# Performance work log

Hardware: AMD Instinct MI355X
Metric: run time of the kernel (lower is better)

The kernel has to match this reference:

```python
import jax, jax.numpy as jnp
import numpy as np
from jax import lax

WS = 32          # region_size
N = WS * WS      # tokens per region = 1024
H = 8            # num_heads
HD = 64          # head_dim
C = H * HD       # dim = 512
B = 8            # num_regions * batch
K = 15           # conv_k
SCALE = HD ** -0.5


def _rel_index():
    # Swin relative position index, computed statically with numpy.
    coords = np.stack(np.meshgrid(np.arange(WS), np.arange(WS), indexing='ij'))  # [2,WS,WS]
    flat = coords.reshape(2, -1)                                                 # [2,N]
    rel = (flat[:, :, None] - flat[:, None, :]).transpose(1, 2, 0)               # [N,N,2]
    rel = rel.copy()
    rel[..., 0] += WS - 1
    rel[..., 1] += WS - 1
    rel[..., 0] *= 2 * WS - 1
    return rel.sum(-1)  # [N,N] int

_REL_IDX = jnp.asarray(_rel_index())


def setup_inputs() -> dict:
    key = jax.random.key(0)
    ks = jax.random.split(key, 6)
    return {
        'x': jax.random.normal(ks[0], (B, N, C), dtype=jnp.float32),
        'w_qkv': jax.random.normal(ks[1], (3 * C, C), dtype=jnp.float32) * 0.02,
        'b_qkv': jnp.zeros((3 * C,), dtype=jnp.float32),
        'w_proj': jax.random.normal(ks[2], (C, C), dtype=jnp.float32) * 0.02,
        'b_proj': jnp.zeros((C,), dtype=jnp.float32),
        'rel_table': jax.random.normal(ks[3], ((2 * WS - 1) ** 2, H), dtype=jnp.float32) * 0.02,
        'pe_w': jax.random.normal(ks[4], (H, 1, K, 1), dtype=jnp.float32) * 0.02,
        'pe_b': jnp.zeros((H,), dtype=jnp.float32),
    }


def reference(x, w_qkv, b_qkv, w_proj, b_proj, rel_table, pe_w, pe_b):
    b, n, c = x.shape
    qkv = (x @ w_qkv.T + b_qkv).reshape(b, n, 3, H, HD)
    q = jnp.moveaxis(qkv[:, :, 0], 2, 1)  # [B,H,N,HD]
    k = jnp.moveaxis(qkv[:, :, 1], 2, 1)
    v = jnp.moveaxis(qkv[:, :, 2], 2, 1)

    attn = jnp.einsum('bhnd,bhmd->bhnm', q * SCALE, k)  # [B,H,N,N]

    # depthwise (per-head) conv over the query axis of the attention matrix, kernel (K,1)
    pe = lax.conv_general_dilated(
        attn, pe_w, window_strides=(1, 1), padding=[(K // 2, K // 2), (0, 0)],
        dimension_numbers=('NCHW', 'OIHW', 'NCHW'), feature_group_count=H,
    ) + pe_b[None, :, None, None]
    attn = attn + pe

    # relative position bias gather: [N*N] -> [N,N,H] -> [H,N,N]
    bias = rel_table[_REL_IDX.reshape(-1)].reshape(n, n, H).transpose(2, 0, 1)
    attn = jax.nn.softmax(attn + bias[None], axis=-1)

    out = jnp.einsum('bhnm,bhmd->bnhd', attn, v).reshape(b, n, c)
    return out @ w_proj.T + b_proj
```

## Files before the change

kernel.cpp:

```cpp
#include <hip/hip_runtime.h>

typedef __bf16 bf16x8 __attribute__((ext_vector_type(8)));
typedef float f32x4 __attribute__((ext_vector_type(4)));
typedef unsigned short u16;
typedef unsigned int u32;
typedef unsigned long long u64;

__device__ __forceinline__ float bf2f(u16 x){ u32 u = ((u32)x)<<16; return __builtin_bit_cast(float,u); }
__device__ __forceinline__ u16 f2bf(float f){ u32 u = __builtin_bit_cast(u32,f); u = (u + 0x7fffu + ((u>>16)&1u)) >> 16; return (u16)u; }

__device__ __forceinline__ void glds16(const u16* g, u16* l){
  __builtin_amdgcn_global_load_lds((const __attribute__((address_space(1))) u32*)g,
                                   (__attribute__((address_space(3))) u32*)l, 16, 0, 0);
}

static constexpr float L2E = 1.4426950408889634f;
static constexpr float QSC = 0.125f * 1.4426950408889634f;

__global__ void k_cvtall(const float* __restrict__ x, const float* __restrict__ wq,
                         const float* __restrict__ wp, const float* __restrict__ rt,
                         u16* __restrict__ xo, u16* __restrict__ wqo,
                         u16* __restrict__ wpo, u64* __restrict__ rel2){
  int bid = blockIdx.x;
  if (bid < 5120){
    int i = bid*256 + threadIdx.x;
    const float* s; u16* d; int base;
    if (i < 1048576){ s=x; d=xo; base=0; }
    else if (i < 1245184){ s=wq; d=wqo; base=1048576; }
    else { s=wp; d=wpo; base=1245184; }
    int j = i - base;
    float4 v = reinterpret_cast<const float4*>(s)[j];
    reinterpret_cast<ushort4*>(d)[j] = make_ushort4(f2bf(v.x),f2bf(v.y),f2bf(v.z),f2bf(v.w));
  } else {
    int i = (bid-5120)*256 + threadIdx.x;
    if (i < 31752){
      int h = i / 3969, i2 = i - h*3969;
      u64 v = 0;
      #pragma unroll
      for (int j=0;j<4;j++){
        int idx = i2-3+j;
        u16 bb = 0;
        if (idx >= 0) bb = f2bf(rt[idx*8+h]*L2E);
        v |= (u64)bb << (16*j);
      }
      rel2[i] = v;
    }
  }
}

__device__ __forceinline__ void acc8(float* acc, uint4 v, float w){
  acc[0]=fmaf(w, bf2f((u16)(v.x)),     acc[0]); acc[1]=fmaf(w, bf2f((u16)(v.x>>16)), acc[1]);
  acc[2]=fmaf(w, bf2f((u16)(v.y)),     acc[2]); acc[3]=fmaf(w, bf2f((u16)(v.y>>16)), acc[3]);
  acc[4]=fmaf(w, bf2f((u16)(v.z)),     acc[4]); acc[5]=fmaf(w, bf2f((u16)(v.z>>16)), acc[5]);
  acc[6]=fmaf(w, bf2f((u16)(v.w)),     acc[6]); acc[7]=fmaf(w, bf2f((u16)(v.w>>16)), acc[7]);
}

template<int MODE>
__global__ __launch_bounds__(256) void k_gemm(
  const u16* __restrict__ A, const u16* __restrict__ Bw, const float* __restrict__ bias,
  u16* __restrict__ qo, u16* __restrict__ ko, u16* __restrict__ vo, float* __restrict__ co)
{
  constexpr int K = 512;
  constexpr int BM = (MODE==0) ? 128 : 64;
  constexpr int NX = (MODE==0) ? 12 : 4;
  constexpr int CPX = NX*(8192/BM)/8;
  constexpr int NF = (MODE==0) ? 4 : 2;
  __shared__ __align__(16) u16 lA[3][BM*32];
  __shared__ __align__(16) u16 lB[3][4096];
  const int lin = blockIdx.y*NX + blockIdx.x;
  const int swz = (lin&7)*CPX + (lin>>3);
  const int i0 = (swz/NX)*BM, j0 = (swz%NX)*128;
  const int T = threadIdx.x;
  const int w = T>>6, lane = T&63, g = lane>>4, cl = lane&15;
  const int wr = (MODE==0) ? (w>>1)*64 : 0;
  const int wc = (MODE==0) ? (w&1)*64 : w*32;
  const int sr = T>>2, sk = 8*(T&3);
  f32x4 acc[4][NF];
  #pragma unroll
  for (int a=0;a<4;a++)
    #pragma unroll
    for (int b=0;b<NF;b++) acc[a][b] = (f32x4){0.f,0.f,0.f,0.f};

  auto STAGE = [&](int t, u16* bA, u16* bB){
    glds16(A  + (long)(i0+sr)*K    + t*32 + sk, bA + 8*T);
    if (MODE==0) glds16(A + (long)(i0+64+sr)*K + t*32 + sk, bA + 2048 + 8*T);
    glds16(Bw + (long)(j0+sr)*K    + t*32 + sk, bB + 8*T);
    glds16(Bw + (long)(j0+64+sr)*K + t*32 + sk, bB + 2048 + 8*T);
  };
  STAGE(0, lA[0], lB[0]);
  STAGE(1, lA[1], lB[1]);
  int cur = 0, sb = 2;
  for (int t=0;t<16;t++){
    if (t<15){
      if (MODE==0) asm volatile("s_waitcnt vmcnt(4)" ::: "memory");
      else         asm volatile("s_waitcnt vmcnt(3)" ::: "memory");
    } else {
      asm volatile("s_waitcnt vmcnt(0)" ::: "memory");
    }
    __builtin_amdgcn_s_barrier();
    asm volatile("" ::: "memory");
    if (t<14) STAGE(t+2, lA[sb], lB[sb]);
    const u16* cA = lA[cur];
    const u16* cB = lB[cur];
    bf16x8 af[4], bfr[NF];
    #pragma unroll
    for (int mf=0;mf<4;mf++) af[mf]  = *reinterpret_cast<const bf16x8*>(cA + (wr+16*mf+cl)*32 + 8*g);
    #pragma unroll
    for (int nf=0;nf<NF;nf++) bfr[nf] = *reinterpret_cast<const bf16x8*>(cB + (wc+16*nf+cl)*32 + 8*g);
    __builtin_amdgcn_s_setprio(1);
    #pragma unroll
    for (int mf=0;mf<4;mf++)
      #pragma unroll
      for (int nf=0;nf<NF;nf++)
        acc[mf][nf] = __builtin_amdgcn_mfma_f32_16x16x32_bf16(af[mf], bfr[nf], acc[mf][nf], 0,0,0);
    __builtin_amdgcn_s_setprio(0);
    cur = (cur==2)?0:cur+1;
    sb  = (sb==2)?0:sb+1;
  }

  #pragma unroll
  for (int mf=0;mf<4;mf++){
    #pragma unroll
    for (int nf=0;nf<NF;nf++){
      const int col = j0 + wc + 16*nf + cl;
      const float bb = bias[col];
      const int row0 = i0 + wr + 16*mf + 4*g;
      if (MODE==0){
        const int part = col>>9, h=(col>>6)&7, dd=col&63;
        const int b = row0>>10, n0 = row0&1023, bh = b*8+h;
        if (part==2){
          const int a32 = n0 & ~31, G = (n0>>2)&7;
          const int stb = ((G&3)<<3) | ((G>>2)<<2);
          ushort4 pk = make_ushort4(f2bf(acc[mf][nf][0]+bb), f2bf(acc[mf][nf][1]+bb),
                                    f2bf(acc[mf][nf][2]+bb), f2bf(acc[mf][nf][3]+bb));
          *reinterpret_cast<ushort4*>(vo + ((long)bh*64+dd)*1024 + a32 + stb) = pk;
        } else {
          #pragma unroll
          for (int e=0;e<4;e++){
            float v = acc[mf][nf][e] + bb;
            if (part==0) qo[((long)bh*1024+n0+e)*64+dd] = f2bf(v*QSC);
            else         ko[((long)bh*1024+n0+e)*64+dd] = f2bf(v);
          }
        }
      } else {
        #pragma unroll
        for (int e=0;e<4;e++)
          co[(long)(row0+e)*512 + col] = acc[mf][nf][e] + bb;
      }
    }
  }
}

__global__ __launch_bounds__(512,4) void k_attn(
  const u16* __restrict__ Qp, const u16* __restrict__ Kb, const u16* __restrict__ VT,
  const u64* __restrict__ relT2, const float* __restrict__ pw, u16* __restrict__ Ao)
{
  __shared__ __align__(16) u16 smem[33792];
  const int bid = blockIdx.x;
  const int xcd = bid&7, slot = bid>>3;
  const int bh = xcd*8 + (slot>>3), rb = slot&7;
  const int b = bh>>3, h = bh&7;
  const int T = threadIdx.x, w=T>>6, lane=T&63, g=lane>>4, cl=lane&15;
  const int rowbase = rb*128 + w*16;
  const int qr = rowbase + cl;
  const u16* Qbh = Qp + (long)bh*65536;
  const u16* Kbh = Kb + (long)bh*65536;
  const u16* Vbh = VT + (long)bh*65536;

  auto STAGE = [&](int m0, int bi){
    int row = T>>3, u = T&7, sw = (u ^ (row&7))<<3;
    glds16(Kbh + (m0+row)*64 + sw,         smem + bi*4096 + T*8);
    glds16(Vbh + (long)row*1024 + m0 + sw, smem + 16384 + bi*4096 + T*8);
  };

  bf16x8 qf[2];
  {
    const int rowstart = rb*128 - 8;
    u16* qs = smem + 24576;
    #pragma unroll
    for (int s=0;s<3;s++){
      int idx = s*512 + T;
      if (idx < 1152){
        int row = idx>>3, u = idx&7;
        int gr = rowstart + row; gr = gr < 0 ? 0 : (gr > 1023 ? 1023 : gr);
        glds16(Qbh + gr*64 + ((u ^ (row&7))<<3), qs + idx*8);
      }
    }
    STAGE(0,0); STAGE(64,1);
    asm volatile("s_waitcnt vmcnt(4)" ::: "memory");
    __builtin_amdgcn_s_barrier();
    asm volatile("" ::: "memory");
    float wgt[15];
    #pragma unroll
    for (int t=0;t<15;t++) wgt[t] = pw[h*15+t];
    const int lr = qr - rowstart;
    #pragma unroll
    for (int s2=0;s2<2;s2++){
      const int ub = 4*s2 + g;
      float a[8];
      {
        uint4 cv = *reinterpret_cast<const uint4*>(qs + lr*64 + ((ub ^ (lr&7))<<3));
        a[0]=bf2f((u16)cv.x); a[1]=bf2f((u16)(cv.x>>16));
        a[2]=bf2f((u16)cv.y); a[3]=bf2f((u16)(cv.y>>16));
        a[4]=bf2f((u16)cv.z); a[5]=bf2f((u16)(cv.z>>16));
        a[6]=bf2f((u16)cv.w); a[7]=bf2f((u16)(cv.w>>16));
      }
      #pragma unroll
      for (int t=0;t<15;t++){
        int nn = qr - 7 + t;
        if (nn >= 0 && nn < 1024){
          int lrow = lr - 7 + t;
          uint4 v = *reinterpret_cast<const uint4*>(qs + lrow*64 + ((ub ^ (lrow&7))<<3));
          acc8(a, v, wgt[t]);
        }
      }
      bf16x8 qq;
      #pragma unroll
      for (int j=0;j<8;j++) qq[j] = (__bf16)a[j];
      qf[s2] = qq;
    }
    asm volatile("s_waitcnt vmcnt(0)" ::: "memory");
    __builtin_amdgcn_s_barrier();
    asm volatile("" ::: "memory");
  }

  const int rt = (qr>>5)*63 + (qr&31) + 1984;
  const u64* relTh = relT2 + h*3969;
  float lsum = 0.f;
  f32x4 oacc[4];
  #pragma unroll
  for (int c=0;c<4;c++) oacc[c] = (f32x4){0.f,0.f,0.f,0.f};

  auto QK = [&](const char* kb, f32x4 (&sacc)[4]){
    #pragma unroll
    for (int c=0;c<4;c++) sacc[c] = (f32x4){0.f,0.f,0.f,0.f};
    #pragma unroll
    for (int c=0;c<4;c++){
      const int r = 16*c + cl, rs = r&7;
      const char* kr = kb + r*128;
      bf16x8 kf0 = *reinterpret_cast<const bf16x8*>(kr + ((g    ^rs)<<4));
      bf16x8 kf1 = *reinterpret_cast<const bf16x8*>(kr + (((4+g)^rs)<<4));
      sacc[c] = __builtin_amdgcn_mfma_f32_16x16x32_bf16(kf0, qf[0], sacc[c],0,0,0);
      sacc[c] = __builtin_amdgcn_mfma_f32_16x16x32_bf16(kf1, qf[1], sacc[c],0,0,0);
    }
  };
  auto RELLOAD = [&](int t, u64 (&rx)[4]){
    #pragma unroll
    for (int c=0;c<4;c++){
      const int kk = (t<<6) + 16*c + 4*g;
      rx[c] = relTh[rt - ((kk>>5)*63 + (kk&31))];
    }
  };
  auto SMPV = [&](const char* vb, f32x4 (&sacc)[4], u64 (&rx)[4]){
    float p[4][4];
    #pragma unroll
    for (int c=0;c<4;c++){
      const u32 lo = (u32)rx[c], hi = (u32)(rx[c]>>32);
      const float b0 = __builtin_bit_cast(float, hi & 0xffff0000u);
      const float b1 = __builtin_bit_cast(float, hi << 16);
      const float b2 = __builtin_bit_cast(float, lo & 0xffff0000u);
      const float b3 = __builtin_bit_cast(float, lo << 16);
      p[c][0] = __builtin_amdgcn_exp2f(sacc[c][0] + b0);
      p[c][1] = __builtin_amdgcn_exp2f(sacc[c][1] + b1);
      p[c][2] = __builtin_amdgcn_exp2f(sacc[c][2] + b2);
      p[c][3] = __builtin_amdgcn_exp2f(sacc[c][3] + b3);
    }
    #pragma unroll
    for (int c=0;c<4;c++) lsum += (p[c][0]+p[c][1]) + (p[c][2]+p[c][3]);
    bf16x8 pa0, pa1;
    #pragma unroll
    for (int e=0;e<4;e++){
      pa0[e]   = (__bf16)p[0][e];  pa0[4+e] = (__bf16)p[1][e];
      pa1[e]   = (__bf16)p[2][e];  pa1[4+e] = (__bf16)p[3][e];
    }
    #pragma unroll
    for (int ks=0;ks<2;ks++){
      const bf16x8 pa = ks ? pa1 : pa0;
      #pragma unroll
      for (int c2=0;c2<4;c2++){
        const int dd = 16*c2 + cl, dsw = dd&7;
        bf16x8 vf = *reinterpret_cast<const bf16x8*>(vb + dd*128 + (((4*ks+g)^dsw)<<4));
        oacc[c2] = __builtin_amdgcn_mfma_f32_16x16x32_bf16(pa, vf, oacc[c2],0,0,0);
      }
    }
  };

  f32x4 saccA[4], saccB[4];
  u64 rxA[4], rxB[4];

  for (int p=0;p<8;p++){
    const int t0 = 2*p, t1 = t0+1;
    if (p<7){ STAGE((t0+2)<<6, (t0+2)&3); STAGE((t1+2)<<6, (t1+2)&3); }
    asm volatile("" ::: "memory");
    RELLOAD(t0, rxA);
    RELLOAD(t1, rxB);
    __builtin_amdgcn_s_setprio(1);
    QK((const char*)(smem + (t0&3)*4096), saccA);
    QK((const char*)(smem + (t1&3)*4096), saccB);
    SMPV((const char*)(smem + 16384 + (t0&3)*4096), saccA, rxA);
    SMPV((const char*)(smem + 16384 + (t1&3)*4096), saccB, rxB);
    __builtin_amdgcn_s_setprio(0);
    if (p<7){
      asm volatile("s_waitcnt vmcnt(0)" ::: "memory");
      __builtin_amdgcn_s_barrier();
      asm volatile("" ::: "memory");
    }
  }

  lsum += __shfl_xor(lsum, 16, 64);
  lsum += __shfl_xor(lsum, 32, 64);
  #pragma unroll
  for (int e=0;e<4;e++){
    float inv = 1.0f/__shfl(lsum, 4*g+e, 64);
    const long orow = (long)b*1024 + rowbase + 4*g + e;
    #pragma unroll
    for (int c2=0;c2<4;c2++)
      Ao[orow*512 + h*64 + 16*c2 + cl] = f2bf(oacc[c2][e]*inv);
  }
}

extern "C" void kernel_launch(void* const* d_in, const int* in_sizes, int n_in,
                              void* d_out, int out_size, void* d_ws, size_t ws_size,
                              hipStream_t stream)
{
  const float* x         = (const float*)d_in[0];
  const float* w_qkv     = (const float*)d_in[1];
  const float* b_qkv     = (const float*)d_in[2];
  const float* w_proj    = (const float*)d_in[3];
  const float* b_proj    = (const float*)d_in[4];
  const float* rel_table = (const float*)d_in[5];
  const float* pe_w      = (const float*)d_in[6];
  (void)in_sizes; (void)n_in; (void)out_size; (void)ws_size;

  u16* ws    = (u16*)d_ws;
  u16* x_bf  = ws;
  u16* wq_bf = x_bf  + 4194304;
  u16* wp_bf = wq_bf + 786432;
  u16* q_bf  = wp_bf + 262144;
  u16* k_bf  = q_bf  + 4194304;
  u16* vt_bf = k_bf  + 4194304;
  u16* ao_bf = vt_bf + 4194304;
  u64* relT2 = (u64*)(ao_bf + 4194304);

  k_cvtall<<<5245,256,0,stream>>>(x, w_qkv, w_proj, rel_table, x_bf, wq_bf, wp_bf, relT2);
  k_gemm<0><<<dim3(12,64),256,0,stream>>>(x_bf, wq_bf, b_qkv, q_bf, k_bf, vt_bf, nullptr);
  k_attn<<<512,512,0,stream>>>(q_bf, k_bf, vt_bf, relT2, pe_w, ao_bf);
  k_gemm<1><<<dim3(4,128),256,0,stream>>>(ao_bf, wp_bf, b_proj, nullptr, nullptr, nullptr, (float*)d_out);
}
```

Measured before the change: 76.33 us.

## Load K and V fragments directly from global memory instead of LDS staging

Removes the LDS double/quad-buffered staging of K and V tiles and the per-iteration barriers, having each wave read its MFMA fragments straight from global memory (L2/cache) per 64-key tile. Shared memory shrinks to just the Q halo buffer, which could raise occupancy and drops the synchronization cost. The trade-off is that the eight waves of a block now each fetch the same K/V data redundantly through the cache, and global load latency is no longer hidden by an explicit software prefetch pipeline.

```diff
diff --git a/kernel.cpp b/kernel.cpp
--- a/kernel.cpp
+++ b/kernel.cpp
@@ -155,7 +155,7 @@
   const u16* __restrict__ Qp, const u16* __restrict__ Kb, const u16* __restrict__ VT,
   const u64* __restrict__ relT2, const float* __restrict__ pw, u16* __restrict__ Ao)
 {
-  __shared__ __align__(16) u16 smem[33792];
+  __shared__ __align__(16) u16 qs[9216];
   const int bid = blockIdx.x;
   const int xcd = bid&7, slot = bid>>3;
   const int bh = xcd*8 + (slot>>3), rb = slot&7;
@@ -167,16 +167,9 @@
   const u16* Kbh = Kb + (long)bh*65536;
   const u16* Vbh = VT + (long)bh*65536;
 
-  auto STAGE = [&](int m0, int bi){
-    int row = T>>3, u = T&7, sw = (u ^ (row&7))<<3;
-    glds16(Kbh + (m0+row)*64 + sw,         smem + bi*4096 + T*8);
-    glds16(Vbh + (long)row*1024 + m0 + sw, smem + 16384 + bi*4096 + T*8);
-  };
-
   bf16x8 qf[2];
   {
     const int rowstart = rb*128 - 8;
-    u16* qs = smem + 24576;
     #pragma unroll
     for (int s=0;s<3;s++){
       int idx = s*512 + T;
@@ -186,8 +179,7 @@
         glds16(Qbh + gr*64 + ((u ^ (row&7))<<3), qs + idx*8);
       }
     }
-    STAGE(0,0); STAGE(64,1);
-    asm volatile("s_waitcnt vmcnt(4)" ::: "memory");
+    asm volatile("s_waitcnt vmcnt(0)" ::: "memory");
     __builtin_amdgcn_s_barrier();
     asm volatile("" ::: "memory");
     float wgt[15];
@@ -219,9 +211,6 @@
       for (int j=0;j<8;j++) qq[j] = (__bf16)a[j];
       qf[s2] = qq;
     }
-    asm volatile("s_waitcnt vmcnt(0)" ::: "memory");
-    __builtin_amdgcn_s_barrier();
-    asm volatile("" ::: "memory");
   }
 
   const int rt = (qr>>5)*63 + (qr&31) + 1984;
@@ -231,27 +220,36 @@
   #pragma unroll
   for (int c=0;c<4;c++) oacc[c] = (f32x4){0.f,0.f,0.f,0.f};
 
-  auto QK = [&](const char* kb, f32x4 (&sacc)[4]){
-    #pragma unroll
-    for (int c=0;c<4;c++) sacc[c] = (f32x4){0.f,0.f,0.f,0.f};
+  for (int t=0;t<16;t++){
+    const int m0 = t<<6;
+    bf16x8 kf[4][2];
     #pragma unroll
     for (int c=0;c<4;c++){
-      const int r = 16*c + cl, rs = r&7;
-      const char* kr = kb + r*128;
-      bf16x8 kf0 = *reinterpret_cast<const bf16x8*>(kr + ((g    ^rs)<<4));
-      bf16x8 kf1 = *reinterpret_cast<const bf16x8*>(kr + (((4+g)^rs)<<4));
-      sacc[c] = __builtin_amdgcn_mfma_f32_16x16x32_bf16(kf0, qf[0], sacc[c],0,0,0);
-      sacc[c] = __builtin_amdgcn_mfma_f32_16x16x32_bf16(kf1, qf[1], sacc[c],0,0,0);
-    }
-  };
-  auto RELLOAD = [&](int t, u64 (&rx)[4]){
+      const u16* Kr = Kbh + (m0 + 16*c + cl)*64;
+      kf[c][0] = *reinterpret_cast<const bf16x8*>(Kr + 8*g);
+      kf[c][1] = *reinterpret_cast<const bf16x8*>(Kr + 32 + 8*g);
+    }
+    bf16x8 vf[2][4];
+    #pragma unroll
+    for (int ks=0;ks<2;ks++)
+      #pragma unroll
+      for (int c2=0;c2<4;c2++)
+        vf[ks][c2] = *reinterpret_cast<const bf16x8*>(Vbh + (16*c2+cl)*1024 + m0 + 32*ks + 8*g);
+    u64 rx[4];
     #pragma unroll
     for (int c=0;c<4;c++){
-      const int kk = (t<<6) + 16*c + 4*g;
+      const int kk = m0 + 16*c + 4*g;
       rx[c] = relTh[rt - ((kk>>5)*63 + (kk&31))];
     }
-  };
-  auto SMPV = [&](const char* vb, f32x4 (&sacc)[4], u64 (&rx)[4]){
+    f32x4 sacc[4];
+    __builtin_amdgcn_s_setprio(1);
+    #pragma unroll
+    for (int c=0;c<4;c++){
+      sacc[c] = (f32x4){0.f,0.f,0.f,0.f};
+      sacc[c] = __builtin_amdgcn_mfma_f32_16x16x32_bf16(kf[c][0], qf[0], sacc[c],0,0,0);
+      sacc[c] = __builtin_amdgcn_mfma_f32_16x16x32_bf16(kf[c][1], qf[1], sacc[c],0,0,0);
+    }
+    __builtin_amdgcn_s_setprio(0);
     float p[4][4];
     #pragma unroll
     for (int c=0;c<4;c++){
@@ -273,38 +271,15 @@
       pa0[e]   = (__bf16)p[0][e];  pa0[4+e] = (__bf16)p[1][e];
       pa1[e]   = (__bf16)p[2][e];  pa1[4+e] = (__bf16)p[3][e];
     }
+    __builtin_amdgcn_s_setprio(1);
     #pragma unroll
     for (int ks=0;ks<2;ks++){
       const bf16x8 pa = ks ? pa1 : pa0;
       #pragma unroll
-      for (int c2=0;c2<4;c2++){
-        const int dd = 16*c2 + cl, dsw = dd&7;
-        bf16x8 vf = *reinterpret_cast<const bf16x8*>(vb + dd*128 + (((4*ks+g)^dsw)<<4));
-        oacc[c2] = __builtin_amdgcn_mfma_f32_16x16x32_bf16(pa, vf, oacc[c2],0,0,0);
-      }
-    }
-  };
-
-  f32x4 saccA[4], saccB[4];
-  u64 rxA[4], rxB[4];
-
-  for (int p=0;p<8;p++){
-    const int t0 = 2*p, t1 = t0+1;
-    if (p<7){ STAGE((t0+2)<<6, (t0+2)&3); STAGE((t1+2)<<6, (t1+2)&3); }
-    asm volatile("" ::: "memory");
-    RELLOAD(t0, rxA);
-    RELLOAD(t1, rxB);
-    __builtin_amdgcn_s_setprio(1);
-    QK((const char*)(smem + (t0&3)*4096), saccA);
-    QK((const char*)(smem + (t1&3)*4096), saccB);
-    SMPV((const char*)(smem + 16384 + (t0&3)*4096), saccA, rxA);
-    SMPV((const char*)(smem + 16384 + (t1&3)*4096), saccB, rxB);
+      for (int c2=0;c2<4;c2++)
+        oacc[c2] = __builtin_amdgcn_mfma_f32_16x16x32_bf16(pa, vf[ks][c2], oacc[c2],0,0,0);
+    }
     __builtin_amdgcn_s_setprio(0);
-    if (p<7){
-      asm volatile("s_waitcnt vmcnt(0)" ::: "memory");
-      __builtin_amdgcn_s_barrier();
-      asm volatile("" ::: "memory");
-    }
   }
 
   lsum += __shfl_xor(lsum, 16, 64);
```

Result: slower. 169.0 us (+121.4%).
